# Optimization experiments

Hardware: AMD Instinct MI355X
Metric: run time of the kernel (lower is better)

The kernel has to match this reference:

```python
import jax, jax.numpy as jnp
import numpy as np

B, N, D, H = 4, 4096, 1024, 16
DK = D // H


def setup_inputs() -> dict:
    key = jax.random.key(0)
    ks = jax.random.split(key, 11)
    s = 0.02  # small init scale for weights
    return {
        "query": jax.random.normal(ks[0], (B, N, D), jnp.float32),
        "key": jax.random.normal(ks[1], (B, N, D), jnp.float32),
        "value": jax.random.normal(ks[2], (B, N, D), jnp.float32),
        "Wq": jax.random.normal(ks[3], (D, D), jnp.float32) * s,
        "bq": jax.random.normal(ks[4], (D,), jnp.float32) * s,
        "Wk": jax.random.normal(ks[5], (D, D), jnp.float32) * s,
        "bk": jax.random.normal(ks[6], (D,), jnp.float32) * s,
        "Wv": jax.random.normal(ks[7], (D, D), jnp.float32) * s,
        "bv": jax.random.normal(ks[8], (D,), jnp.float32) * s,
        "Wo": jax.random.normal(ks[9], (D, D), jnp.float32) * s,
        "bo": jax.random.normal(ks[10], (D,), jnp.float32) * s,
    }


def reference(query, key, value, Wq, bq, Wk, bk, Wv, bv, Wo, bo):
    b, n, d = query.shape
    h, dk = H, d // H

    def proj(x, W, bias):
        # torch Linear: y = x @ W.T + b ; then split heads -> [b,h,n,dk]
        y = x @ W.T + bias
        return y.reshape(b, n, h, dk).transpose(0, 2, 1, 3)

    q = proj(query, Wq, bq)
    k = proj(key, Wk, bk)
    v = proj(value, Wv, bv)

    # linear attention (Efficient Attention, arXiv:1812.01243)
    q = jax.nn.softmax(q, axis=-1) * (1.0 / np.sqrt(dk).astype(np.float32))
    k = jax.nn.softmax(k, axis=-2)  # softmax over sequence dim
    ctx = jnp.einsum('bhnd,bhne->bhde', k, v)   # [b,h,dk,dk]
    out = jnp.einsum('bhnd,bhde->bhne', q, ctx)  # [b,h,n,dk]

    out = out.transpose(0, 2, 1, 3).reshape(b, n, d)
    return out @ Wo.T + bo
```

## Files before the change

### kernel.cpp

```cpp
#include <hip/hip_runtime.h>
#include <hip/hip_bf16.h>

#define B_ 4
#define N_ 4096
#define D_ 1024
#define H_ 16

typedef __attribute__((ext_vector_type(4))) float f32x4;
typedef __attribute__((ext_vector_type(8))) short s16x8;
typedef __attribute__((ext_vector_type(4))) unsigned int u32x4;

__device__ __forceinline__ ushort f2bf(float f) {
  union { float f; unsigned u; } v; v.f = f;
  unsigned u = v.u;
  return (ushort)((u + 0x7fffu + ((u >> 16) & 1u)) >> 16);
}

__device__ __forceinline__ void gld16(const ushort* g, ushort* lds_base) {
  __builtin_amdgcn_global_load_lds(
      (const __attribute__((address_space(1))) unsigned int*)g,
      (__attribute__((address_space(3))) unsigned int*)lds_base, 16, 0, 0);
}

__device__ __forceinline__ unsigned cvtpk(float lo, float hi) {
  unsigned r;
  asm("v_cvt_pk_bf16_f32 %0, %1, %2" : "=v"(r) : "v"(lo), "v"(hi));
  return r;
}

__global__ void conv_w_kernel(const float* __restrict__ w0, const float* __restrict__ w1,
                              const float* __restrict__ w2, const float* __restrict__ w3,
                              ushort* __restrict__ dst) {
  const int z = blockIdx.z;
  const float* src = z == 0 ? w0 : z == 1 ? w1 : z == 2 ? w2 : w3;
  ushort* d = dst + (long)z * (D_ * D_);
  const long i0 = ((long)blockIdx.x * 256 + threadIdx.x) * 8;
  const long STR = (long)128 * 256 * 8;
#pragma unroll
  for (int u = 0; u < 4; ++u) {
    f32x4 a = *(const f32x4*)(src + i0 + u * STR);
    f32x4 b = *(const f32x4*)(src + i0 + u * STR + 4);
    s16x8 o;
    o[0] = (short)f2bf(a[0]); o[1] = (short)f2bf(a[1]); o[2] = (short)f2bf(a[2]); o[3] = (short)f2bf(a[3]);
    o[4] = (short)f2bf(b[0]); o[5] = (short)f2bf(b[1]); o[6] = (short)f2bf(b[2]); o[7] = (short)f2bf(b[3]);
    *(s16x8*)(d + i0 + u * STR) = o;
  }
}

template <int EPI, bool AFP32>
__device__ __forceinline__ void gemm_body(
    const void* __restrict__ Av, const ushort* __restrict__ Bm,
    void* __restrict__ Cv, const float* __restrict__ bias, float* __restrict__ kpart,
    int m0, int n0) {
  __shared__ ushort As[8192];
  __shared__ ushort Bs[8192];
  const int N = 1024;
  const int tid = threadIdx.x;
  const int lane = tid & 63;
  const int wave = tid >> 6;
  const int fl = lane & 15, fh = lane >> 4;
  const int wm = wave >> 2, wn = wave & 3;
  f32x4 acc[8][4] = {};

  const int fro = (fh ^ ((fl >> 1) & 3)) * 8;
  const int rmb = (wm * 128 + fl) * 32;
  const int rnb = (wn * 64 + fl) * 32;

  const int brow = tid >> 2;
  const int bslot = ((tid & 3) ^ ((brow >> 1) & 3)) * 8;
  const ushort* Bsrc0 = Bm + (long)(n0 + brow) * 1024 + bslot;
  const ushort* Bsrc1 = Bm + (long)(n0 + brow + 128) * 1024 + bslot;

  const ushort* Ab = (const ushort*)Av;
  const ushort* Asrc0 = AFP32 ? nullptr : (Ab + (long)(m0 + brow) * 1024 + bslot);
  const ushort* Asrc1 = AFP32 ? nullptr : (Ab + (long)(m0 + brow + 128) * 1024 + bslot);

  const int ar = tid >> 1, ch = tid & 1;
  const float* apA = AFP32 ? ((const float*)Av + (long)(m0 + ar) * 1024 + ch * 16) : nullptr;
  const int aw0 = ar * 32 + (((ch * 2) ^ ((ar >> 1) & 3)) * 8);
  const int aw1 = ar * 32 + (((ch * 2 + 1) ^ ((ar >> 1) & 3)) * 8);

#define ISSUE_B(T) do { \
    gld16(Bsrc0 + (T) * 32, Bs + tid * 8); \
    gld16(Bsrc1 + (T) * 32, Bs + tid * 8 + 4096); } while (0)
#define ISSUE_A16(T) do { \
    gld16(Asrc0 + (T) * 32, As + tid * 8); \
    gld16(Asrc1 + (T) * 32, As + tid * 8 + 4096); } while (0)
#define ISSUE_P(T, S) do { \
    S##0 = *(const f32x4*)(apA + (T) * 32); \
    S##1 = *(const f32x4*)(apA + (T) * 32 + 4); \
    S##2 = *(const f32x4*)(apA + (T) * 32 + 8); \
    S##3 = *(const f32x4*)(apA + (T) * 32 + 12); } while (0)
#define CVT_WRITE(S) do { \
    u32x4 _w0, _w1; \
    _w0[0] = cvtpk(S##0[0], S##0[1]); _w0[1] = cvtpk(S##0[2], S##0[3]); \
    _w0[2] = cvtpk(S##1[0], S##1[1]); _w0[3] = cvtpk(S##1[2], S##1[3]); \
    _w1[0] = cvtpk(S##2[0], S##2[1]); _w1[1] = cvtpk(S##2[2], S##2[3]); \
    _w1[2] = cvtpk(S##3[0], S##3[1]); _w1[3] = cvtpk(S##3[2], S##3[3]); \
    *(u32x4*)(As + aw0) = _w0; \
    *(u32x4*)(As + aw1) = _w1; } while (0)
#define MFMA_STEP() do { \
    s16x8 fb[4]; \
    _Pragma("unroll") for (int j = 0; j < 4; ++j) \
      fb[j] = *(const s16x8*)(Bs + rnb + j * 512 + fro); \
    _Pragma("unroll") for (int i = 0; i < 8; ++i) { \
      s16x8 fa = *(const s16x8*)(As + rmb + i * 512 + fro); \
      _Pragma("unroll") for (int j = 0; j < 4; ++j) \
        acc[i][j] = __builtin_amdgcn_mfma_f32_16x16x32_bf16(fa, fb[j], acc[i][j], 0, 0, 0); \
    } } while (0)

  if constexpr (AFP32) {
    f32x4 qa0, qa1, qa2, qa3, qb0, qb1, qb2, qb3;
    ISSUE_P(0, qa);
#pragma unroll 1
    for (int t = 0; t < 32; t += 2) {
      CVT_WRITE(qa);
      ISSUE_P(t + 1, qb);
      ISSUE_B(t);
      __syncthreads();
      MFMA_STEP();
      __syncthreads();
      CVT_WRITE(qb);
      if (t < 30) ISSUE_P(t + 2, qa);
      ISSUE_B(t + 1);
      __syncthreads();
      MFMA_STEP();
      __syncthreads();
    }
  } else {
#pragma unroll 1
    for (int t = 0; t < 32; ++t) {
      ISSUE_A16(t);
      ISSUE_B(t);
      __syncthreads();
      MFMA_STEP();
      __syncthreads();
    }
  }
#undef ISSUE_B
#undef ISSUE_A16
#undef ISSUE_P
#undef CVT_WRITE
#undef MFMA_STEP

  if constexpr (EPI == 0) {
    ushort* C = (ushort*)Cv;
#pragma unroll
    for (int j = 0; j < 4; ++j) {
      int col = n0 + wn * 64 + j * 16 + fl;
#pragma unroll
      for (int i = 0; i < 8; ++i)
#pragma unroll
        for (int r = 0; r < 4; ++r) {
          int row = m0 + wm * 128 + i * 16 + fh * 4 + r;
          C[(long)row * N + col] = f2bf(acc[i][j][r]);
        }
    }
  } else if constexpr (EPI == 1) {
    ushort* C = (ushort*)Cv;
    float bcol[4];
#pragma unroll
    for (int j = 0; j < 4; ++j) bcol[j] = bias[n0 + wn * 64 + j * 16 + fl];
#pragma unroll
    for (int i = 0; i < 8; ++i)
#pragma unroll
      for (int r = 0; r < 4; ++r) {
        float v[4];
#pragma unroll
        for (int j = 0; j < 4; ++j) v[j] = acc[i][j][r] + bcol[j];
        float m = fmaxf(fmaxf(v[0], v[1]), fmaxf(v[2], v[3]));
#pragma unroll
        for (int o = 1; o <= 8; o <<= 1) m = fmaxf(m, __shfl_xor(m, o));
        float e[4], s = 0.f;
#pragma unroll
        for (int j = 0; j < 4; ++j) { e[j] = __expf(v[j] - m); s += e[j]; }
#pragma unroll
        for (int o = 1; o <= 8; o <<= 1) s += __shfl_xor(s, o);
        float sc = 0.125f / s;
        int row = m0 + wm * 128 + i * 16 + fh * 4 + r;
#pragma unroll
        for (int j = 0; j < 4; ++j)
          C[(long)row * N + n0 + wn * 64 + j * 16 + fl] = f2bf(e[j] * sc);
      }
  } else if constexpr (EPI == 2) {
    ushort* C = (ushort*)Cv;
    float csum[4] = {};
#pragma unroll
    for (int j = 0; j < 4; ++j) {
      int col = n0 + wn * 64 + j * 16 + fl;
#pragma unroll
      for (int i = 0; i < 8; ++i)
#pragma unroll
        for (int r = 0; r < 4; ++r) {
          int row = m0 + wm * 128 + i * 16 + fh * 4 + r;
          float e = __expf(acc[i][j][r]);
          csum[j] += e;
          C[(long)row * N + col] = f2bf(e);
        }
    }
#pragma unroll
    for (int j = 0; j < 4; ++j) {
#pragma unroll
      for (int o = 16; o <= 32; o <<= 1) csum[j] += __shfl_xor(csum[j], o);
    }
    if (fh == 0) {
      int b = m0 >> 12;
      int chunk = ((m0 & 4095) >> 7) + wm;
#pragma unroll
      for (int j = 0; j < 4; ++j)
        kpart[(long)b * 32768 + (long)chunk * 1024 + n0 + wn * 64 + j * 16 + fl] = csum[j];
    }
  } else {
    float* C = (float*)Cv;
#pragma unroll
    for (int j = 0; j < 4; ++j) {
      int col = n0 + wn * 64 + j * 16 + fl;
      float bv = bias[col];
#pragma unroll
      for (int i = 0; i < 8; ++i)
#pragma unroll
        for (int r = 0; r < 4; ++r) {
          int row = m0 + wm * 128 + i * 16 + fh * 4 + r;
          C[(long)row * N + col] = acc[i][j][r] + bv;
        }
    }
  }
}

__global__ __launch_bounds__(512, 2) void gemm_q(const float* __restrict__ A,
                                                 const ushort* __restrict__ Bm,
                                                 ushort* __restrict__ C,
                                                 const float* __restrict__ bias) {
  gemm_body<1, true>(A, Bm, C, bias, nullptr, blockIdx.x * 256, blockIdx.y * 256);
}
__global__ __launch_bounds__(512, 2) void gemm_k(const float* __restrict__ A,
                                                 const ushort* __restrict__ Bm,
                                                 ushort* __restrict__ C,
                                                 float* __restrict__ kpart) {
  gemm_body<2, true>(A, Bm, C, nullptr, kpart, blockIdx.x * 256, blockIdx.y * 256);
}
__global__ __launch_bounds__(512, 2) void gemm_v(const float* __restrict__ A,
                                                 const ushort* __restrict__ Bm,
                                                 ushort* __restrict__ C) {
  gemm_body<0, true>(A, Bm, C, nullptr, nullptr, blockIdx.x * 256, blockIdx.y * 256);
}
__global__ __launch_bounds__(512, 2) void gemm_o(const ushort* __restrict__ A,
                                                 const ushort* __restrict__ Bm,
                                                 float* __restrict__ C,
                                                 const float* __restrict__ bias) {
  const int z = blockIdx.z;
  gemm_body<3, false>(A + (long)z * 4096 * 1024, Bm + (long)z * 1024 * 1024,
                      C + (long)z * 4096 * 1024, bias, nullptr,
                      blockIdx.x * 256, blockIdx.y * 256);
}

__global__ void ksm2_kernel(const float* __restrict__ kpart, float* __restrict__ colinv) {
  int idx = blockIdx.x * 256 + threadIdx.x;
  int b = idx >> 10, d = idx & 1023;
  float s = 0.f;
  for (int c = 0; c < 32; ++c) s += kpart[(long)b * 32768 + (long)c * 1024 + d];
  colinv[idx] = 1.0f / s;
}

__global__ __launch_bounds__(256, 2) void ctx_partial_kernel(
    const ushort* __restrict__ Ksm, const ushort* __restrict__ Vp, float* __restrict__ part) {
  __shared__ ushort Ks[128 * 64];
  __shared__ ushort Vs[128 * 64];
  const int chunk = blockIdx.x;
  const int bh = blockIdx.y;
  const int b = bh >> 4, h = bh & 15;
  const int tid = threadIdx.x, wave = tid >> 6, lane = tid & 63;
  const int fl = lane & 15, fh = lane >> 4;
  f32x4 acc[4] = {};
  for (int t = 0; t < 4; ++t) {
    const long base = ((long)(b * N_ + chunk * 512 + t * 128)) * D_ + h * 64;
    __syncthreads();
#pragma unroll
    for (int i = 0; i < 4; ++i) {
      int c = i * 256 + tid;
      int r = c >> 3, k8 = (c & 7) * 8;
      ushort* lk = Ks + (long)(i * 256 + wave * 64) * 8;
      ushort* lv = Vs + (long)(i * 256 + wave * 64) * 8;
      gld16(Ksm + base + (long)r * D_ + k8, lk);
      gld16(Vp + base + (long)r * D_ + k8, lv);
    }
    __syncthreads();
#pragma unroll
    for (int s = 0; s < 4; ++s) {
      s16x8 fa;
#pragma unroll
      for (int j = 0; j < 8; ++j)
        fa[j] = (short)Ks[(s * 32 + fh * 8 + j) * 64 + wave * 16 + fl];
#pragma unroll
      for (int jt = 0; jt < 4; ++jt) {
        s16x8 fb;
#pragma unroll
        for (int j = 0; j < 8; ++j)
          fb[j] = (short)Vs[(s * 32 + fh * 8 + j) * 64 + jt * 16 + fl];
        acc[jt] = __builtin_amdgcn_mfma_f32_16x16x32_bf16(fa, fb, acc[jt], 0, 0, 0);
      }
    }
  }
  float* dst = part + ((long)chunk * 64 + bh) * 4096;
#pragma unroll
  for (int jt = 0; jt < 4; ++jt)
#pragma unroll
    for (int r = 0; r < 4; ++r)
      dst[(wave * 16 + fh * 4 + r) * 64 + jt * 16 + fl] = acc[jt][r];
}

__global__ void ctx_reduce_kernel(const float* __restrict__ part, const float* __restrict__ bv,
                                  const float* __restrict__ colinv, ushort* __restrict__ ctxb) {
  int idx = blockIdx.x * 256 + threadIdx.x;
  int e = idx & 63;
  int dk = (idx >> 6) & 63;
  int h = (idx >> 12) & 15;
  int b = idx >> 16;
  float s = 0.f;
#pragma unroll
  for (int c = 0; c < 8; ++c) s += part[(long)c * 262144 + idx];
  ctxb[idx] = f2bf(s * colinv[b * 1024 + h * 64 + dk] + bv[h * 64 + e]);
}

__global__ __launch_bounds__(256, 2) void mb_kernel(
    const ushort* __restrict__ Wob, const ushort* __restrict__ ctxb, ushort* __restrict__ Mb) {
  const int o0 = blockIdx.x * 64, h = blockIdx.y, b = blockIdx.z;
  const int tid = threadIdx.x, wave = tid >> 6, lane = tid & 63;
  const int fl = lane & 15, fh = lane >> 4;
  const ushort* ctxh = ctxb + ((long)(b * 16 + h)) * 4096;
  f32x4 acc[4] = {};
#pragma unroll
  for (int s = 0; s < 2; ++s) {
    s16x8 fa = *(const s16x8*)(Wob + (long)(o0 + wave * 16 + fl) * D_ + h * 64 + s * 32 + fh * 8);
#pragma unroll
    for (int jt = 0; jt < 4; ++jt) {
      s16x8 fb = *(const s16x8*)(ctxh + (long)(jt * 16 + fl) * 64 + s * 32 + fh * 8);
      acc[jt] = __builtin_amdgcn_mfma_f32_16x16x32_bf16(fa, fb, acc[jt], 0, 0, 0);
    }
  }
  ushort* dst = Mb + (long)b * (D_ * D_);
#pragma unroll
  for (int jt = 0; jt < 4; ++jt)
#pragma unroll
    for (int r = 0; r < 4; ++r)
      dst[(long)(o0 + wave * 16 + fh * 4 + r) * D_ + h * 64 + jt * 16 + fl] = f2bf(acc[jt][r]);
}

extern "C" void kernel_launch(void* const* d_in, const int* in_sizes, int n_in,
                              void* d_out, int out_size, void* d_ws, size_t ws_size,
                              hipStream_t stream) {
  const float* q_in = (const float*)d_in[0];
  const float* k_in = (const float*)d_in[1];
  const float* v_in = (const float*)d_in[2];
  const float* Wq = (const float*)d_in[3];
  const float* bq = (const float*)d_in[4];
  const float* Wk = (const float*)d_in[5];
  const float* Wv = (const float*)d_in[7];
  const float* bv = (const float*)d_in[8];
  const float* Wo = (const float*)d_in[9];
  const float* bo = (const float*)d_in[10];

  char* ws = (char*)d_ws;
  ushort* Wb = (ushort*)(ws + 0);
  ushort* Qp = (ushort*)(ws + 8388608);
  ushort* Kp = (ushort*)(ws + 41943040);
  ushort* Vp = (ushort*)(ws + 75497472);
  float* kpart = (float*)(ws + 109051904);
  float* colinv = (float*)(ws + 109576192);
  float* ctxpart = (float*)(ws + 109592576);
  ushort* ctxb = (ushort*)(ws + 117981184);
  ushort* Mb = (ushort*)(ws + 118505472);

  ushort* Wbq = Wb;
  ushort* Wbk = Wb + 1048576;
  ushort* Wbv = Wb + 2097152;
  ushort* Wbo = Wb + 3145728;

  conv_w_kernel<<<dim3(128, 1, 4), 256, 0, stream>>>(Wq, Wk, Wv, Wo, Wb);

  gemm_q<<<dim3(64, 4), 512, 0, stream>>>(q_in, Wbq, Qp, bq);
  gemm_k<<<dim3(64, 4), 512, 0, stream>>>(k_in, Wbk, Kp, kpart);
  gemm_v<<<dim3(64, 4), 512, 0, stream>>>(v_in, Wbv, Vp);

  ksm2_kernel<<<16, 256, 0, stream>>>(kpart, colinv);

  ctx_partial_kernel<<<dim3(8, 64), 256, 0, stream>>>(Kp, Vp, ctxpart);
  ctx_reduce_kernel<<<1024, 256, 0, stream>>>(ctxpart, bv, colinv, ctxb);
  mb_kernel<<<dim3(16, 16, 4), 256, 0, stream>>>(Wbo, ctxb, Mb);

  gemm_o<<<dim3(16, 4, 4), 512, 0, stream>>>(Qp, Mb, (float*)d_out, bo);
}
```

Measured before the change: 318.0 us.

## Shrink GEMM tiles to 64x256 with 256-thread blocks and more CTAs

```diff
diff --git a/kernel.cpp b/kernel.cpp
--- a/kernel.cpp
+++ b/kernel.cpp
@@ -52,93 +52,84 @@
     const void* __restrict__ Av, const ushort* __restrict__ Bm,
     void* __restrict__ Cv, const float* __restrict__ bias, float* __restrict__ kpart,
     int m0, int n0) {
-  __shared__ ushort As[8192];
+  __shared__ ushort As[2048];
   __shared__ ushort Bs[8192];
   const int N = 1024;
   const int tid = threadIdx.x;
   const int lane = tid & 63;
-  const int wave = tid >> 6;
+  const int wn = tid >> 6;
   const int fl = lane & 15, fh = lane >> 4;
-  const int wm = wave >> 2, wn = wave & 3;
-  f32x4 acc[8][4] = {};
+  f32x4 acc[4][4] = {};
+
+  const int br = tid >> 2;
+  const int bsw = (((tid & 3) ^ ((br >> 1) & 3)) * 8);
+  const ushort* Ab = (const ushort*)Av;
+  const ushort* Asrc = AFP32 ? nullptr : (Ab + (long)(m0 + br) * 1024 + bsw);
+
+  const int ar = tid >> 2, sl = tid & 3;
+  const float* apA = AFP32 ? ((const float*)Av + (long)(m0 + ar) * 1024 + sl * 8) : nullptr;
+  const int aw = ar * 32 + ((sl ^ ((ar >> 1) & 3)) * 8);
 
   const int fro = (fh ^ ((fl >> 1) & 3)) * 8;
-  const int rmb = (wm * 128 + fl) * 32;
-  const int rnb = (wn * 64 + fl) * 32;
-
-  const int brow = tid >> 2;
-  const int bslot = ((tid & 3) ^ ((brow >> 1) & 3)) * 8;
-  const ushort* Bsrc0 = Bm + (long)(n0 + brow) * 1024 + bslot;
-  const ushort* Bsrc1 = Bm + (long)(n0 + brow + 128) * 1024 + bslot;
-
-  const ushort* Ab = (const ushort*)Av;
-  const ushort* Asrc0 = AFP32 ? nullptr : (Ab + (long)(m0 + brow) * 1024 + bslot);
-  const ushort* Asrc1 = AFP32 ? nullptr : (Ab + (long)(m0 + brow + 128) * 1024 + bslot);
-
-  const int ar = tid >> 1, ch = tid & 1;
-  const float* apA = AFP32 ? ((const float*)Av + (long)(m0 + ar) * 1024 + ch * 16) : nullptr;
-  const int aw0 = ar * 32 + (((ch * 2) ^ ((ar >> 1) & 3)) * 8);
-  const int aw1 = ar * 32 + (((ch * 2 + 1) ^ ((ar >> 1) & 3)) * 8);
-
-#define ISSUE_B(T) do { \
-    gld16(Bsrc0 + (T) * 32, Bs + tid * 8); \
-    gld16(Bsrc1 + (T) * 32, Bs + tid * 8 + 4096); } while (0)
-#define ISSUE_A16(T) do { \
-    gld16(Asrc0 + (T) * 32, As + tid * 8); \
-    gld16(Asrc1 + (T) * 32, As + tid * 8 + 4096); } while (0)
+
+  f32x4 qa0, qa1, qb0, qb1;
+
+#define GLD_B(T) do { \
+    _Pragma("unroll") for (int i = 0; i < 4; ++i) { \
+      int c = tid + i * 256; \
+      int row = c >> 2; \
+      int sw = (((c & 3) ^ ((row >> 1) & 3)) * 8); \
+      gld16(Bm + (long)(n0 + row) * 1024 + (T) * 32 + sw, Bs + c * 8); \
+    } } while (0)
+#define GLD_A16(T) do { gld16(Asrc + (T) * 32, As + tid * 8); } while (0)
 #define ISSUE_P(T, S) do { \
     S##0 = *(const f32x4*)(apA + (T) * 32); \
-    S##1 = *(const f32x4*)(apA + (T) * 32 + 4); \
-    S##2 = *(const f32x4*)(apA + (T) * 32 + 8); \
-    S##3 = *(const f32x4*)(apA + (T) * 32 + 12); } while (0)
+    S##1 = *(const f32x4*)(apA + (T) * 32 + 4); } while (0)
 #define CVT_WRITE(S) do { \
-    u32x4 _w0, _w1; \
-    _w0[0] = cvtpk(S##0[0], S##0[1]); _w0[1] = cvtpk(S##0[2], S##0[3]); \
-    _w0[2] = cvtpk(S##1[0], S##1[1]); _w0[3] = cvtpk(S##1[2], S##1[3]); \
-    _w1[0] = cvtpk(S##2[0], S##2[1]); _w1[1] = cvtpk(S##2[2], S##2[3]); \
-    _w1[2] = cvtpk(S##3[0], S##3[1]); _w1[3] = cvtpk(S##3[2], S##3[3]); \
-    *(u32x4*)(As + aw0) = _w0; \
-    *(u32x4*)(As + aw1) = _w1; } while (0)
+    u32x4 _w; \
+    _w[0] = cvtpk(S##0[0], S##0[1]); _w[1] = cvtpk(S##0[2], S##0[3]); \
+    _w[2] = cvtpk(S##1[0], S##1[1]); _w[3] = cvtpk(S##1[2], S##1[3]); \
+    *(u32x4*)(As + aw) = _w; } while (0)
 #define MFMA_STEP() do { \
-    s16x8 fb[4]; \
+    s16x8 fa[4], fb[4]; \
+    _Pragma("unroll") for (int i = 0; i < 4; ++i) \
+      fa[i] = *(const s16x8*)(As + (i * 16 + fl) * 32 + fro); \
     _Pragma("unroll") for (int j = 0; j < 4; ++j) \
-      fb[j] = *(const s16x8*)(Bs + rnb + j * 512 + fro); \
-    _Pragma("unroll") for (int i = 0; i < 8; ++i) { \
-      s16x8 fa = *(const s16x8*)(As + rmb + i * 512 + fro); \
+      fb[j] = *(const s16x8*)(Bs + (wn * 64 + j * 16 + fl) * 32 + fro); \
+    _Pragma("unroll") for (int i = 0; i < 4; ++i) \
       _Pragma("unroll") for (int j = 0; j < 4; ++j) \
-        acc[i][j] = __builtin_amdgcn_mfma_f32_16x16x32_bf16(fa, fb[j], acc[i][j], 0, 0, 0); \
-    } } while (0)
+        acc[i][j] = __builtin_amdgcn_mfma_f32_16x16x32_bf16(fa[i], fb[j], acc[i][j], 0, 0, 0); \
+    } while (0)
 
   if constexpr (AFP32) {
-    f32x4 qa0, qa1, qa2, qa3, qb0, qb1, qb2, qb3;
     ISSUE_P(0, qa);
 #pragma unroll 1
     for (int t = 0; t < 32; t += 2) {
+      __syncthreads();
+      GLD_B(t);
       CVT_WRITE(qa);
       ISSUE_P(t + 1, qb);
-      ISSUE_B(t);
       __syncthreads();
       MFMA_STEP();
       __syncthreads();
+      GLD_B(t + 1);
       CVT_WRITE(qb);
-      if (t < 30) ISSUE_P(t + 2, qa);
-      ISSUE_B(t + 1);
+      if (t + 2 < 32) ISSUE_P(t + 2, qa);
       __syncthreads();
       MFMA_STEP();
-      __syncthreads();
     }
   } else {
 #pragma unroll 1
     for (int t = 0; t < 32; ++t) {
-      ISSUE_A16(t);
-      ISSUE_B(t);
+      __syncthreads();
+      GLD_A16(t);
+      GLD_B(t);
       __syncthreads();
       MFMA_STEP();
-      __syncthreads();
-    }
-  }
-#undef ISSUE_B
-#undef ISSUE_A16
+    }
+  }
+#undef GLD_B
+#undef GLD_A16
 #undef ISSUE_P
 #undef CVT_WRITE
 #undef MFMA_STEP
@@ -149,10 +140,10 @@
     for (int j = 0; j < 4; ++j) {
       int col = n0 + wn * 64 + j * 16 + fl;
 #pragma unroll
-      for (int i = 0; i < 8; ++i)
+      for (int i = 0; i < 4; ++i)
 #pragma unroll
         for (int r = 0; r < 4; ++r) {
-          int row = m0 + wm * 128 + i * 16 + fh * 4 + r;
+          int row = m0 + i * 16 + fh * 4 + r;
           C[(long)row * N + col] = f2bf(acc[i][j][r]);
         }
     }
@@ -162,7 +153,7 @@
 #pragma unroll
     for (int j = 0; j < 4; ++j) bcol[j] = bias[n0 + wn * 64 + j * 16 + fl];
 #pragma unroll
-    for (int i = 0; i < 8; ++i)
+    for (int i = 0; i < 4; ++i)
 #pragma unroll
       for (int r = 0; r < 4; ++r) {
         float v[4];
@@ -177,7 +168,7 @@
 #pragma unroll
         for (int o = 1; o <= 8; o <<= 1) s += __shfl_xor(s, o);
         float sc = 0.125f / s;
-        int row = m0 + wm * 128 + i * 16 + fh * 4 + r;
+        int row = m0 + i * 16 + fh * 4 + r;
 #pragma unroll
         for (int j = 0; j < 4; ++j)
           C[(long)row * N + n0 + wn * 64 + j * 16 + fl] = f2bf(e[j] * sc);
@@ -189,10 +180,10 @@
     for (int j = 0; j < 4; ++j) {
       int col = n0 + wn * 64 + j * 16 + fl;
 #pragma unroll
-      for (int i = 0; i < 8; ++i)
+      for (int i = 0; i < 4; ++i)
 #pragma unroll
         for (int r = 0; r < 4; ++r) {
-          int row = m0 + wm * 128 + i * 16 + fh * 4 + r;
+          int row = m0 + i * 16 + fh * 4 + r;
           float e = __expf(acc[i][j][r]);
           csum[j] += e;
           C[(long)row * N + col] = f2bf(e);
@@ -205,10 +196,10 @@
     }
     if (fh == 0) {
       int b = m0 >> 12;
-      int chunk = ((m0 & 4095) >> 7) + wm;
+      int chunk = (m0 & 4095) >> 6;
 #pragma unroll
       for (int j = 0; j < 4; ++j)
-        kpart[(long)b * 32768 + (long)chunk * 1024 + n0 + wn * 64 + j * 16 + fl] = csum[j];
+        kpart[(long)b * 65536 + (long)chunk * 1024 + n0 + wn * 64 + j * 16 + fl] = csum[j];
     }
   } else {
     float* C = (float*)Cv;
@@ -217,48 +208,48 @@
       int col = n0 + wn * 64 + j * 16 + fl;
       float bv = bias[col];
 #pragma unroll
-      for (int i = 0; i < 8; ++i)
+      for (int i = 0; i < 4; ++i)
 #pragma unroll
         for (int r = 0; r < 4; ++r) {
-          int row = m0 + wm * 128 + i * 16 + fh * 4 + r;
+          int row = m0 + i * 16 + fh * 4 + r;
           C[(long)row * N + col] = acc[i][j][r] + bv;
         }
     }
   }
 }
 
-__global__ __launch_bounds__(512, 2) void gemm_q(const float* __restrict__ A,
+__global__ __launch_bounds__(256, 2) void gemm_q(const float* __restrict__ A,
                                                  const ushort* __restrict__ Bm,
                                                  ushort* __restrict__ C,
                                                  const float* __restrict__ bias) {
-  gemm_body<1, true>(A, Bm, C, bias, nullptr, blockIdx.x * 256, blockIdx.y * 256);
-}
-__global__ __launch_bounds__(512, 2) void gemm_k(const float* __restrict__ A,
+  gemm_body<1, true>(A, Bm, C, bias, nullptr, blockIdx.x * 64, blockIdx.y * 256);
+}
+__global__ __launch_bounds__(256, 2) void gemm_k(const float* __restrict__ A,
                                                  const ushort* __restrict__ Bm,
                                                  ushort* __restrict__ C,
                                                  float* __restrict__ kpart) {
-  gemm_body<2, true>(A, Bm, C, nullptr, kpart, blockIdx.x * 256, blockIdx.y * 256);
-}
-__global__ __launch_bounds__(512, 2) void gemm_v(const float* __restrict__ A,
+  gemm_body<2, true>(A, Bm, C, nullptr, kpart, blockIdx.x * 64, blockIdx.y * 256);
+}
+__global__ __launch_bounds__(256, 2) void gemm_v(const float* __restrict__ A,
                                                  const ushort* __restrict__ Bm,
                                                  ushort* __restrict__ C) {
-  gemm_body<0, true>(A, Bm, C, nullptr, nullptr, blockIdx.x * 256, blockIdx.y * 256);
-}
-__global__ __launch_bounds__(512, 2) void gemm_o(const ushort* __restrict__ A,
+  gemm_body<0, true>(A, Bm, C, nullptr, nullptr, blockIdx.x * 64, blockIdx.y * 256);
+}
+__global__ __launch_bounds__(256, 2) void gemm_o(const ushort* __restrict__ A,
                                                  const ushort* __restrict__ Bm,
                                                  float* __restrict__ C,
                                                  const float* __restrict__ bias) {
   const int z = blockIdx.z;
   gemm_body<3, false>(A + (long)z * 4096 * 1024, Bm + (long)z * 1024 * 1024,
                       C + (long)z * 4096 * 1024, bias, nullptr,
-                      blockIdx.x * 256, blockIdx.y * 256);
+                      blockIdx.x * 64, blockIdx.y * 256);
 }
 
 __global__ void ksm2_kernel(const float* __restrict__ kpart, float* __restrict__ colinv) {
   int idx = blockIdx.x * 256 + threadIdx.x;
   int b = idx >> 10, d = idx & 1023;
   float s = 0.f;
-  for (int c = 0; c < 32; ++c) s += kpart[(long)b * 32768 + (long)c * 1024 + d];
+  for (int c = 0; c < 64; ++c) s += kpart[(long)b * 65536 + (long)c * 1024 + d];
   colinv[idx] = 1.0f / s;
 }
 
@@ -366,10 +357,10 @@
   ushort* Kp = (ushort*)(ws + 41943040);
   ushort* Vp = (ushort*)(ws + 75497472);
   float* kpart = (float*)(ws + 109051904);
-  float* colinv = (float*)(ws + 109576192);
-  float* ctxpart = (float*)(ws + 109592576);
-  ushort* ctxb = (ushort*)(ws + 117981184);
-  ushort* Mb = (ushort*)(ws + 118505472);
+  float* colinv = (float*)(ws + 110100480);
+  float* ctxpart = (float*)(ws + 110116864);
+  ushort* ctxb = (ushort*)(ws + 118505472);
+  ushort* Mb = (ushort*)(ws + 119029760);
 
   ushort* Wbq = Wb;
   ushort* Wbk = Wb + 1048576;
@@ -378,9 +369,9 @@
 
   conv_w_kernel<<<dim3(128, 1, 4), 256, 0, stream>>>(Wq, Wk, Wv, Wo, Wb);
 
-  gemm_q<<<dim3(64, 4), 512, 0, stream>>>(q_in, Wbq, Qp, bq);
-  gemm_k<<<dim3(64, 4), 512, 0, stream>>>(k_in, Wbk, Kp, kpart);
-  gemm_v<<<dim3(64, 4), 512, 0, stream>>>(v_in, Wbv, Vp);
+  gemm_q<<<dim3(256, 4), 256, 0, stream>>>(q_in, Wbq, Qp, bq);
+  gemm_k<<<dim3(256, 4), 256, 0, stream>>>(k_in, Wbk, Kp, kpart);
+  gemm_v<<<dim3(256, 4), 256, 0, stream>>>(v_in, Wbv, Vp);
 
   ksm2_kernel<<<16, 256, 0, stream>>>(kpart, colinv);
 
@@ -388,5 +379,5 @@
   ctx_reduce_kernel<<<1024, 256, 0, stream>>>(ctxpart, bv, colinv, ctxb);
   mb_kernel<<<dim3(16, 16, 4), 256, 0, stream>>>(Wbo, ctxb, Mb);
 
-  gemm_o<<<dim3(16, 4, 4), 512, 0, stream>>>(Qp, Mb, (float*)d_out, bo);
-}
+  gemm_o<<<dim3(64, 4, 4), 256, 0, stream>>>(Qp, Mb, (float*)d_out, bo);
+}
```

New measurement: 339.4 us. 6.7% more time.
